# Kernel optimization log

Hardware: AMD Instinct MI355X
Metric: run time of the kernel (lower is better)

The kernel has to match this reference:

```python
import jax, jax.numpy as jnp
import numpy as np

TOPK = 30  # from init_kwargs


def setup_inputs() -> dict:
    key = jax.random.key(0)
    k1, k2, k3 = jax.random.split(key, 3)
    BH, N, D = 32, 2048, 64  # (batch*heads, seq_len, head_dim)
    return {
        "q": jax.random.normal(k1, (BH, N, D), dtype=jnp.float32),
        "k": jax.random.normal(k2, (BH, N, D), dtype=jnp.float32),
        "v": jax.random.normal(k3, (BH, N, D), dtype=jnp.float32),
        "B": 2048,          # == seq_len N (used for mask shape in original)
        "num_heads": 8,     # unused by the math, kept for signature parity
    }


def reference(q, k, v, B, num_heads):
    # scores: [BH, N, N]  (torch.bmm(q, k.transpose(1,2)))
    scores = jnp.einsum('bnd,bmd->bnm', q, k)
    # scale=None and attn_mask=None in the default call -> both branches skipped
    BH, N, _ = scores.shape
    # top-k per row, scatter 1.0 into a zero mask (faithful to torch.scatter_)
    _, idx = jax.lax.top_k(scores, TOPK)                      # [BH, N, TOPK]
    bi = jnp.arange(BH)[:, None, None]
    ri = jnp.arange(N)[None, :, None]
    keep = jnp.zeros((BH, N, N), dtype=bool).at[bi, ri, idx].set(True)
    # masked softmax over last axis (dim=2)
    masked = jnp.where(keep, scores, -jnp.inf)
    attn = jax.nn.softmax(masked, axis=-1)
    # dropout p=0.0 -> identity
    context = jnp.einsum('bnm,bmd->bnd', attn, v)
    return context, attn
```

## Files before the change

kernel.cpp:

```cpp
#include <hip/hip_runtime.h>
#include <hip/hip_bf16.h>

#define BHn 32
#define Nn 2048
#define Dn 64
#define KSEL 30
#define CAP 112
#define RB 128
#define CT 64
#define ZTH 1.80f

typedef short bf16x8 __attribute__((ext_vector_type(8)));
typedef float f32x4 __attribute__((ext_vector_type(4)));
typedef unsigned long long u64;

__device__ __forceinline__ unsigned ford(float x) {
  unsigned b = __float_as_uint(x);
  return (b & 0x80000000u) ? ~b : (b | 0x80000000u);
}
__device__ __forceinline__ float unford(unsigned u) {
  unsigned b = (u & 0x80000000u) ? (u & 0x7fffffffu) : ~u;
  return __uint_as_float(b);
}
__device__ __forceinline__ u64 umax64(u64 a, u64 b) { return a > b ? a : b; }

__device__ __forceinline__ void split2(float a, float b, ushort2& hi, ushort2& lo) {
  __hip_bfloat162 h = __float22bfloat162_rn(make_float2(a, b));
  union { __hip_bfloat162 v; ushort2 u; } ch; ch.v = h;
  hi = ch.u;
  float2 hf = __bfloat1622float2(h);
  __hip_bfloat162 l = __float22bfloat162_rn(make_float2(a - hf.x, b - hf.y));
  union { __hip_bfloat162 v; ushort2 u; } cl; cl.v = l;
  lo = cl.u;
}

__global__ __launch_bounds__(256, 3) void score_cand(
    const float* __restrict__ q, const float* __restrict__ k,
    u64* __restrict__ cand, unsigned* __restrict__ counts) {
  __shared__ ushort qh[RB][64], ql[RB][64];
  __shared__ ushort kh[CT][64], kl[CT][64];
  __shared__ unsigned ccnt[RB];
  __shared__ float tf[RB];

  const int t = threadIdx.x;
  const int bid = blockIdx.x;
  const int bh = (bid & 7) * 4 + ((bid >> 3) & 3);
  const int rb = bid >> 5;
  const int lane = t & 63, w = t >> 6;
  const int m16 = lane & 15, quad = lane >> 4;

  const float* qb = q + ((size_t)bh * Nn + rb * RB) * Dn;
  const float* kb = k + (size_t)bh * Nn * Dn;
  const size_t growbase = (size_t)bh * Nn + (size_t)rb * RB;

#pragma unroll
  for (int i = 0; i < 8; ++i) {
    int c = t + 256 * i;
    int row = c >> 4, f4 = c & 15;
    float4 a = *(const float4*)(qb + row * Dn + f4 * 4);
    int sp = (((f4 >> 1) ^ (row & 7)) << 1) | (f4 & 1);
    ushort2 h0, l0, h1, l1;
    split2(a.x, a.y, h0, l0);
    split2(a.z, a.w, h1, l1);
    *(ushort4*)&qh[row][sp * 4] = make_ushort4(h0.x, h0.y, h1.x, h1.y);
    *(ushort4*)&ql[row][sp * 4] = make_ushort4(l0.x, l0.y, l1.x, l1.y);
  }
  if (t < RB) {
    const float* qr = qb + t * Dn;
    float ss = 0.f;
#pragma unroll
    for (int i = 0; i < 16; ++i) {
      float4 a = *(const float4*)(qr + i * 4);
      ss = fmaf(a.x, a.x, ss); ss = fmaf(a.y, a.y, ss);
      ss = fmaf(a.z, a.z, ss); ss = fmaf(a.w, a.w, ss);
    }
    tf[t] = ZTH * sqrtf(ss);
    ccnt[t] = 0u;
  }

  unsigned tfr[2][4];
  float4 pre[4];
#pragma unroll
  for (int i = 0; i < 4; ++i) {
    int c = t + 256 * i;
    pre[i] = *(const float4*)(kb + (size_t)(c >> 4) * Dn + (c & 15) * 4);
  }
  __syncthreads();

#pragma unroll
  for (int mt = 0; mt < 2; ++mt)
#pragma unroll
    for (int rg = 0; rg < 4; ++rg)
      tfr[mt][rg] = ford(tf[w * 32 + mt * 16 + quad * 4 + rg]);

  for (int ct = 0; ct < Nn / CT; ++ct) {
#pragma unroll
    for (int i = 0; i < 4; ++i) {
      int c = t + 256 * i;
      int row = c >> 4, f4 = c & 15;
      float4 a = pre[i];
      int sp = (((f4 >> 1) ^ (row & 7)) << 1) | (f4 & 1);
      ushort2 h0, l0, h1, l1;
      split2(a.x, a.y, h0, l0);
      split2(a.z, a.w, h1, l1);
      *(ushort4*)&kh[row][sp * 4] = make_ushort4(h0.x, h0.y, h1.x, h1.y);
      *(ushort4*)&kl[row][sp * 4] = make_ushort4(l0.x, l0.y, l1.x, l1.y);
    }
    __syncthreads();

    if (ct + 1 < Nn / CT) {
#pragma unroll
      for (int i = 0; i < 4; ++i) {
        int c = t + 256 * i;
        pre[i] = *(const float4*)(kb + (size_t)((ct + 1) * CT + (c >> 4)) * Dn + (c & 15) * 4);
      }
    }

    f32x4 acc[2][4];
#pragma unroll
    for (int mt = 0; mt < 2; ++mt)
#pragma unroll
      for (int nt = 0; nt < 4; ++nt) acc[mt][nt] = (f32x4){0.f, 0.f, 0.f, 0.f};

#pragma unroll
    for (int ks = 0; ks < 2; ++ks) {
      bf16x8 aH[2], aL[2], bH[4], bL[4];
#pragma unroll
      for (int mt = 0; mt < 2; ++mt) {
        int r = w * 32 + mt * 16 + m16;
        int ch = (ks * 4 + quad) ^ (r & 7);
        aH[mt] = *(const bf16x8*)&qh[r][ch * 8];
        aL[mt] = *(const bf16x8*)&ql[r][ch * 8];
      }
#pragma unroll
      for (int nt = 0; nt < 4; ++nt) {
        int rr = nt * 16 + m16;
        int ch = (ks * 4 + quad) ^ (rr & 7);
        bH[nt] = *(const bf16x8*)&kh[rr][ch * 8];
        bL[nt] = *(const bf16x8*)&kl[rr][ch * 8];
      }
#pragma unroll
      for (int mt = 0; mt < 2; ++mt)
#pragma unroll
        for (int nt = 0; nt < 4; ++nt) {
          acc[mt][nt] = __builtin_amdgcn_mfma_f32_16x16x32_bf16(aL[mt], bH[nt], acc[mt][nt], 0, 0, 0);
          acc[mt][nt] = __builtin_amdgcn_mfma_f32_16x16x32_bf16(aH[mt], bL[nt], acc[mt][nt], 0, 0, 0);
          acc[mt][nt] = __builtin_amdgcn_mfma_f32_16x16x32_bf16(aH[mt], bH[nt], acc[mt][nt], 0, 0, 0);
        }
    }

#pragma unroll
    for (int mt = 0; mt < 2; ++mt)
#pragma unroll
      for (int rg = 0; rg < 4; ++rg) {
        unsigned tk = tfr[mt][rg];
        int rl = w * 32 + mt * 16 + quad * 4 + rg;
#pragma unroll
        for (int nt = 0; nt < 4; ++nt) {
          float s = acc[mt][nt][rg];
          unsigned fk = ford(s);
          if (fk > tk) {
            unsigned pos = atomicAdd(&ccnt[rl], 1u);
            if (pos < CAP) {
              int col = ct * CT + nt * 16 + m16;
              cand[(growbase + rl) * CAP + pos] =
                  ((u64)fk << 32) | (unsigned)(2047 - col);
            }
          }
        }
      }
    __syncthreads();
  }
  if (t < RB) counts[growbase + t] = ccnt[t];
}

__global__ __launch_bounds__(256) void select_fill(
    u64* __restrict__ cand, const unsigned* __restrict__ counts,
    const float* __restrict__ v, float* __restrict__ ctx,
    float* __restrict__ attn, unsigned* __restrict__ flags) {
  __shared__ float lrow[4 * Nn];
  __shared__ u64 scr[4][CAP];
  const int t = threadIdx.x;
  const int lane = t & 63, wv = t >> 6;
  const size_t row0 = (size_t)blockIdx.x * 4;
  const size_t gr = row0 + wv;
  const int bh = (int)(gr >> 11);

#pragma unroll
  for (int i = 0; i < 8; ++i)
    *(f32x4*)&lrow[i * 1024 + t * 4] = (f32x4){0.f, 0.f, 0.f, 0.f};

  const int C = (int)counts[gr];
  const bool bad = (C < KSEL) || (C > CAP);
  if (lane == 0) flags[gr] = bad ? 1u : 0u;

  if (!bad) {
    u64* sw_ = scr[wv];
    for (int p = lane; p < C; p += 64) sw_[p] = cand[gr * CAP + p];

    const int slots = (C + 63) >> 6;
    u64 mykey[2] = {0ull, 0ull};
    int rk[2] = {CAP, CAP};
    float es[2] = {0.f, 0.f};
    u64 mymax = 0ull;
#pragma unroll
    for (int tt = 0; tt < 2; ++tt) {
      if (tt < slots) {
        int p = lane + 64 * tt;
        mykey[tt] = (p < C) ? sw_[p] : 0ull;
        mymax = umax64(mymax, mykey[tt]);
      }
    }
#pragma unroll
    for (int off = 32; off; off >>= 1) mymax = umax64(mymax, __shfl_xor(mymax, off));
    const float mrow = unford((unsigned)(mymax >> 32));

#pragma unroll 1
    for (int tt = 0; tt < slots; ++tt) {
      int r = 0;
      u64 me = mykey[tt];
      for (int jj = 0; jj < C; ++jj) r += (sw_[jj] > me);
      rk[tt] = r;
    }
    float z = 0.f;
#pragma unroll
    for (int tt = 0; tt < 2; ++tt) {
      int p = lane + 64 * tt;
      bool sel = (tt < slots) && (p < C) && (rk[tt] < KSEL);
      es[tt] = sel ? __expf(unford((unsigned)(mykey[tt] >> 32)) - mrow) : 0.f;
      z += es[tt];
    }
#pragma unroll
    for (int off = 32; off; off >>= 1) z += __shfl_xor(z, off);
    const float invZ = 1.f / z;

#pragma unroll
    for (int tt = 0; tt < 2; ++tt) {
      int p = lane + 64 * tt;
      if (tt < slots && p < C && rk[tt] < KSEL) {
        float wt = es[tt] * invZ;
        int col = 2047 - (int)(mykey[tt] & 0xffffffffu);
        u64 e = ((u64)__float_as_uint(wt) << 32) | (unsigned)col;
        sw_[rk[tt]] = e;
        lrow[wv * Nn + col] = wt;
      }
    }
    const float* vb = v + (size_t)bh * Nn * Dn;
    float a = 0.f;
#pragma unroll
    for (int p = 0; p < KSEL; ++p) {
      u64 e = sw_[p];
      a = fmaf(__uint_as_float((unsigned)(e >> 32)), vb[(e & 0x7ffull) * Dn + lane], a);
    }
    ctx[gr * Dn + lane] = a;
  }
  __syncthreads();

  float* ab = attn + row0 * Nn;
#pragma unroll
  for (int i = 0; i < 8; ++i) {
    f32x4 vv = *(const f32x4*)&lrow[i * 1024 + t * 4];
    __builtin_nontemporal_store(vv, (f32x4*)(ab + i * 1024 + t * 4));
  }
}

__global__ __launch_bounds__(256) void repair_rows(
    const float* __restrict__ q, const float* __restrict__ k,
    const float* __restrict__ v, float* __restrict__ ctx,
    float* __restrict__ attn, const unsigned* __restrict__ flags) {
  __shared__ float sc2[Nn];
  __shared__ u64 red[256];
  __shared__ float qrow[Dn];
  __shared__ int selc[KSEL];
  __shared__ float selv[KSEL];
  __shared__ float zsh;
  __shared__ unsigned flagbuf[256];

  const int t = threadIdx.x;
  const int base = blockIdx.x * 256;
  flagbuf[t] = flags[base + t];
  __syncthreads();

  for (int i = 0; i < 256; ++i) {
    if (flagbuf[i] == 0u) continue;
    const int gr = base + i;
    const int bh = gr >> 11;
    if (t < Dn) qrow[t] = q[(size_t)gr * Dn + t];
    __syncthreads();
    const float* kb = k + (size_t)bh * Nn * Dn;
#pragma unroll
    for (int j = 0; j < 8; ++j) {
      int col = t + 256 * j;
      float s = 0.f;
      for (int d = 0; d < Dn; d += 4) {
        float4 kk = *(const float4*)(kb + (size_t)col * Dn + d);
        s = fmaf(qrow[d], kk.x, s);
        s = fmaf(qrow[d + 1], kk.y, s);
        s = fmaf(qrow[d + 2], kk.z, s);
        s = fmaf(qrow[d + 3], kk.w, s);
      }
      sc2[col] = s;
    }
    __syncthreads();
    for (int p = 0; p < KSEL; ++p) {
      u64 best = 0ull;
#pragma unroll
      for (int j = 0; j < 8; ++j) {
        int col = t + 256 * j;
        u64 kk = ((u64)ford(sc2[col]) << 32) | (unsigned)(2047 - col);
        best = umax64(best, kk);
      }
      red[t] = best;
      __syncthreads();
      for (int off = 128; off; off >>= 1) {
        if (t < off) red[t] = umax64(red[t], red[t + off]);
        __syncthreads();
      }
      if (t == 0) {
        u64 b = red[0];
        int col = 2047 - (int)(b & 0xffffffffu);
        selc[p] = col;
        selv[p] = unford((unsigned)(b >> 32));
        sc2[col] = -3.4e38f;
      }
      __syncthreads();
    }
    if (t == 0) {
      float m = selv[0], zz = 0.f;
      for (int p = 0; p < KSEL; ++p) zz += __expf(selv[p] - m);
      zsh = 1.f / zz;
    }
    __syncthreads();
    if (t < KSEL)
      attn[(size_t)gr * Nn + selc[t]] = __expf(selv[t] - selv[0]) * zsh;
    if (t < Dn) {
      const float* vb = v + (size_t)bh * Nn * Dn;
      float a = 0.f;
      for (int p = 0; p < KSEL; ++p)
        a = fmaf(__expf(selv[p] - selv[0]) * zsh, vb[(size_t)selc[p] * Dn + t], a);
      ctx[(size_t)gr * Dn + t] = a;
    }
    __syncthreads();
  }
}

extern "C" void kernel_launch(void* const* d_in, const int* in_sizes, int n_in,
                              void* d_out, int out_size, void* d_ws,
                              size_t ws_size, hipStream_t stream) {
  const float* q = (const float*)d_in[0];
  const float* k = (const float*)d_in[1];
  const float* v = (const float*)d_in[2];
  float* out = (float*)d_out;
  float* ctx = out;
  float* attn = out + (size_t)BHn * Nn * Dn;

  unsigned* counts = (unsigned*)d_ws;
  unsigned* flags = counts + (size_t)BHn * Nn;
  u64* cand = (u64*)((char*)d_ws + (size_t)BHn * Nn * 8);

  score_cand<<<dim3(BHn * Nn / RB), 256, 0, stream>>>(q, k, cand, counts);
  select_fill<<<dim3(BHn * Nn / 4), 256, 0, stream>>>(cand, counts, v, ctx, attn, flags);
  repair_rows<<<dim3(BHn * Nn / 256), 256, 0, stream>>>(q, k, v, ctx, attn, flags);
}
```

Measured before the change: 803.8 us.

## Fuse candidate scoring and top-k selection into one kernel with LDS candidate buffers

Merges the score/candidate kernel with the select-and-fill kernel, so candidates stay in shared memory and are never written to or read back from global workspace. Q fragments are held in registers instead of LDS. The row block shrinks to 64 and the 4 waves are split 2x2 over rows and columns. The threshold and capacity change (ZTH 1.90, CAP 92), and the attention row is written as zeros followed by scattered nontemporal stores of the weights. The risks are lower occupancy from the larger LDS candidate array, twice as many K reloads per row, an ordering dependency between the zero and weight stores guarded by a waitcnt, and possibly more rows sent to the repair path.

```diff
diff --git a/kernel.cpp b/kernel.cpp
--- a/kernel.cpp
+++ b/kernel.cpp
@@ -5,10 +5,10 @@
 #define Nn 2048
 #define Dn 64
 #define KSEL 30
-#define CAP 112
-#define RB 128
+#define CAP 92
+#define RB 64
 #define CT 64
-#define ZTH 1.80f
+#define ZTH 1.90f
 
 typedef short bf16x8 __attribute__((ext_vector_type(8)));
 typedef float f32x4 __attribute__((ext_vector_type(4)));
@@ -34,11 +34,22 @@
   lo = cl.u;
 }
 
-__global__ __launch_bounds__(256, 3) void score_cand(
+__device__ __forceinline__ void pack8(float4 x0, float4 x1, bf16x8& hi, bf16x8& lo) {
+  ushort2 h0, l0, h1, l1, h2, l2, h3, l3;
+  split2(x0.x, x0.y, h0, l0); split2(x0.z, x0.w, h1, l1);
+  split2(x1.x, x1.y, h2, l2); split2(x1.z, x1.w, h3, l3);
+  hi = (bf16x8){(short)h0.x, (short)h0.y, (short)h1.x, (short)h1.y,
+                (short)h2.x, (short)h2.y, (short)h3.x, (short)h3.y};
+  lo = (bf16x8){(short)l0.x, (short)l0.y, (short)l1.x, (short)l1.y,
+                (short)l2.x, (short)l2.y, (short)l3.x, (short)l3.y};
+}
+
+__global__ __launch_bounds__(256, 2) void score_select(
     const float* __restrict__ q, const float* __restrict__ k,
-    u64* __restrict__ cand, unsigned* __restrict__ counts) {
-  __shared__ ushort qh[RB][64], ql[RB][64];
+    const float* __restrict__ v, float* __restrict__ ctx,
+    float* __restrict__ attn, unsigned* __restrict__ flags) {
   __shared__ ushort kh[CT][64], kl[CT][64];
+  __shared__ u64 candL[RB][CAP];
   __shared__ unsigned ccnt[RB];
   __shared__ float tf[RB];
 
@@ -48,23 +59,23 @@
   const int rb = bid >> 5;
   const int lane = t & 63, w = t >> 6;
   const int m16 = lane & 15, quad = lane >> 4;
+  const int wr = w >> 1, wc = w & 1;
 
   const float* qb = q + ((size_t)bh * Nn + rb * RB) * Dn;
   const float* kb = k + (size_t)bh * Nn * Dn;
   const size_t growbase = (size_t)bh * Nn + (size_t)rb * RB;
 
-#pragma unroll
-  for (int i = 0; i < 8; ++i) {
-    int c = t + 256 * i;
-    int row = c >> 4, f4 = c & 15;
-    float4 a = *(const float4*)(qb + row * Dn + f4 * 4);
-    int sp = (((f4 >> 1) ^ (row & 7)) << 1) | (f4 & 1);
-    ushort2 h0, l0, h1, l1;
-    split2(a.x, a.y, h0, l0);
-    split2(a.z, a.w, h1, l1);
-    *(ushort4*)&qh[row][sp * 4] = make_ushort4(h0.x, h0.y, h1.x, h1.y);
-    *(ushort4*)&ql[row][sp * 4] = make_ushort4(l0.x, l0.y, l1.x, l1.y);
-  }
+  bf16x8 qaH[2][2], qaL[2][2];
+#pragma unroll
+  for (int ks = 0; ks < 2; ++ks)
+#pragma unroll
+    for (int mt = 0; mt < 2; ++mt) {
+      const float* p = qb + (wr * 32 + mt * 16 + m16) * Dn + (ks * 4 + quad) * 8;
+      float4 x0 = *(const float4*)p;
+      float4 x1 = *(const float4*)(p + 4);
+      pack8(x0, x1, qaH[ks][mt], qaL[ks][mt]);
+    }
+
   if (t < RB) {
     const float* qr = qb + t * Dn;
     float ss = 0.f;
@@ -78,7 +89,6 @@
     ccnt[t] = 0u;
   }
 
-  unsigned tfr[2][4];
   float4 pre[4];
 #pragma unroll
   for (int i = 0; i < 4; ++i) {
@@ -87,11 +97,12 @@
   }
   __syncthreads();
 
+  unsigned tfr[2][4];
 #pragma unroll
   for (int mt = 0; mt < 2; ++mt)
 #pragma unroll
     for (int rg = 0; rg < 4; ++rg)
-      tfr[mt][rg] = ford(tf[w * 32 + mt * 16 + quad * 4 + rg]);
+      tfr[mt][rg] = ford(tf[wr * 32 + mt * 16 + quad * 4 + rg]);
 
   for (int ct = 0; ct < Nn / CT; ++ct) {
 #pragma unroll
@@ -116,25 +127,18 @@
       }
     }
 
-    f32x4 acc[2][4];
+    f32x4 acc[2][2];
 #pragma unroll
     for (int mt = 0; mt < 2; ++mt)
 #pragma unroll
-      for (int nt = 0; nt < 4; ++nt) acc[mt][nt] = (f32x4){0.f, 0.f, 0.f, 0.f};
+      for (int nt = 0; nt < 2; ++nt) acc[mt][nt] = (f32x4){0.f, 0.f, 0.f, 0.f};
 
 #pragma unroll
     for (int ks = 0; ks < 2; ++ks) {
-      bf16x8 aH[2], aL[2], bH[4], bL[4];
-#pragma unroll
-      for (int mt = 0; mt < 2; ++mt) {
-        int r = w * 32 + mt * 16 + m16;
-        int ch = (ks * 4 + quad) ^ (r & 7);
-        aH[mt] = *(const bf16x8*)&qh[r][ch * 8];
-        aL[mt] = *(const bf16x8*)&ql[r][ch * 8];
-      }
-#pragma unroll
-      for (int nt = 0; nt < 4; ++nt) {
-        int rr = nt * 16 + m16;
+      bf16x8 bH[2], bL[2];
+#pragma unroll
+      for (int nt = 0; nt < 2; ++nt) {
+        int rr = wc * 32 + nt * 16 + m16;
         int ch = (ks * 4 + quad) ^ (rr & 7);
         bH[nt] = *(const bf16x8*)&kh[rr][ch * 8];
         bL[nt] = *(const bf16x8*)&kl[rr][ch * 8];
@@ -142,10 +146,10 @@
 #pragma unroll
       for (int mt = 0; mt < 2; ++mt)
 #pragma unroll
-        for (int nt = 0; nt < 4; ++nt) {
-          acc[mt][nt] = __builtin_amdgcn_mfma_f32_16x16x32_bf16(aL[mt], bH[nt], acc[mt][nt], 0, 0, 0);
-          acc[mt][nt] = __builtin_amdgcn_mfma_f32_16x16x32_bf16(aH[mt], bL[nt], acc[mt][nt], 0, 0, 0);
-          acc[mt][nt] = __builtin_amdgcn_mfma_f32_16x16x32_bf16(aH[mt], bH[nt], acc[mt][nt], 0, 0, 0);
+        for (int nt = 0; nt < 2; ++nt) {
+          acc[mt][nt] = __builtin_amdgcn_mfma_f32_16x16x32_bf16(qaL[ks][mt], bH[nt], acc[mt][nt], 0, 0, 0);
+          acc[mt][nt] = __builtin_amdgcn_mfma_f32_16x16x32_bf16(qaH[ks][mt], bL[nt], acc[mt][nt], 0, 0, 0);
+          acc[mt][nt] = __builtin_amdgcn_mfma_f32_16x16x32_bf16(qaH[ks][mt], bH[nt], acc[mt][nt], 0, 0, 0);
         }
     }
 
@@ -154,113 +158,103 @@
 #pragma unroll
       for (int rg = 0; rg < 4; ++rg) {
         unsigned tk = tfr[mt][rg];
-        int rl = w * 32 + mt * 16 + quad * 4 + rg;
-#pragma unroll
-        for (int nt = 0; nt < 4; ++nt) {
+        int rl = wr * 32 + mt * 16 + quad * 4 + rg;
+#pragma unroll
+        for (int nt = 0; nt < 2; ++nt) {
           float s = acc[mt][nt][rg];
           unsigned fk = ford(s);
           if (fk > tk) {
             unsigned pos = atomicAdd(&ccnt[rl], 1u);
             if (pos < CAP) {
-              int col = ct * CT + nt * 16 + m16;
-              cand[(growbase + rl) * CAP + pos] =
-                  ((u64)fk << 32) | (unsigned)(2047 - col);
+              int col = ct * CT + wc * 32 + nt * 16 + m16;
+              candL[rl][pos] = ((u64)fk << 32) | (unsigned)(2047 - col);
             }
           }
         }
       }
     __syncthreads();
   }
-  if (t < RB) counts[growbase + t] = ccnt[t];
-}
-
-__global__ __launch_bounds__(256) void select_fill(
-    u64* __restrict__ cand, const unsigned* __restrict__ counts,
-    const float* __restrict__ v, float* __restrict__ ctx,
-    float* __restrict__ attn, unsigned* __restrict__ flags) {
-  __shared__ float lrow[4 * Nn];
-  __shared__ u64 scr[4][CAP];
-  const int t = threadIdx.x;
-  const int lane = t & 63, wv = t >> 6;
-  const size_t row0 = (size_t)blockIdx.x * 4;
-  const size_t gr = row0 + wv;
-  const int bh = (int)(gr >> 11);
-
-#pragma unroll
-  for (int i = 0; i < 8; ++i)
-    *(f32x4*)&lrow[i * 1024 + t * 4] = (f32x4){0.f, 0.f, 0.f, 0.f};
-
-  const int C = (int)counts[gr];
-  const bool bad = (C < KSEL) || (C > CAP);
-  if (lane == 0) flags[gr] = bad ? 1u : 0u;
-
-  if (!bad) {
-    u64* sw_ = scr[wv];
-    for (int p = lane; p < C; p += 64) sw_[p] = cand[gr * CAP + p];
-
-    const int slots = (C + 63) >> 6;
-    u64 mykey[2] = {0ull, 0ull};
-    int rk[2] = {CAP, CAP};
-    float es[2] = {0.f, 0.f};
-    u64 mymax = 0ull;
-#pragma unroll
-    for (int tt = 0; tt < 2; ++tt) {
-      if (tt < slots) {
+
+  const float* vb = v + (size_t)bh * Nn * Dn;
+  for (int i = 0; i < RB / 4; ++i) {
+    const int rl = w * 16 + i;
+    const size_t gr = growbase + rl;
+    const int C = (int)ccnt[rl];
+    const bool bad = (C < KSEL) || (C > CAP);
+    if (lane == 0) flags[gr] = bad ? 1u : 0u;
+    float* ab = attn + gr * (size_t)Nn;
+
+    const f32x4 Z = (f32x4){0.f, 0.f, 0.f, 0.f};
+#pragma unroll
+    for (int jj = 0; jj < 8; ++jj)
+      __builtin_nontemporal_store(Z, (f32x4*)(ab + jj * 256 + lane * 4));
+
+    if (!bad) {
+      u64* sw_ = &candL[rl][0];
+      const int slots = (C + 63) >> 6;
+      u64 mykey[2] = {0ull, 0ull};
+      int rk[2] = {CAP, CAP};
+      float es[2] = {0.f, 0.f};
+      u64 mymax = 0ull;
+#pragma unroll
+      for (int tt = 0; tt < 2; ++tt) {
+        if (tt < slots) {
+          int p = lane + 64 * tt;
+          mykey[tt] = (p < C) ? sw_[p] : 0ull;
+          mymax = umax64(mymax, mykey[tt]);
+        }
+      }
+#pragma unroll
+      for (int off = 32; off; off >>= 1) mymax = umax64(mymax, __shfl_xor(mymax, off));
+      const float mrow = unford((unsigned)(mymax >> 32));
+
+#pragma unroll 1
+      for (int tt = 0; tt < slots; ++tt) {
+        int r = 0;
+        u64 me = mykey[tt];
+        for (int jj = 0; jj < C; ++jj) r += (sw_[jj] > me);
+        rk[tt] = r;
+      }
+      float z = 0.f;
+#pragma unroll
+      for (int tt = 0; tt < 2; ++tt) {
         int p = lane + 64 * tt;
-        mykey[tt] = (p < C) ? sw_[p] : 0ull;
-        mymax = umax64(mymax, mykey[tt]);
-      }
-    }
-#pragma unroll
-    for (int off = 32; off; off >>= 1) mymax = umax64(mymax, __shfl_xor(mymax, off));
-    const float mrow = unford((unsigned)(mymax >> 32));
-
-#pragma unroll 1
-    for (int tt = 0; tt < slots; ++tt) {
-      int r = 0;
-      u64 me = mykey[tt];
-      for (int jj = 0; jj < C; ++jj) r += (sw_[jj] > me);
-      rk[tt] = r;
-    }
-    float z = 0.f;
-#pragma unroll
-    for (int tt = 0; tt < 2; ++tt) {
-      int p = lane + 64 * tt;
-      bool sel = (tt < slots) && (p < C) && (rk[tt] < KSEL);
-      es[tt] = sel ? __expf(unford((unsigned)(mykey[tt] >> 32)) - mrow) : 0.f;
-      z += es[tt];
-    }
-#pragma unroll
-    for (int off = 32; off; off >>= 1) z += __shfl_xor(z, off);
-    const float invZ = 1.f / z;
-
-#pragma unroll
-    for (int tt = 0; tt < 2; ++tt) {
-      int p = lane + 64 * tt;
-      if (tt < slots && p < C && rk[tt] < KSEL) {
-        float wt = es[tt] * invZ;
-        int col = 2047 - (int)(mykey[tt] & 0xffffffffu);
-        u64 e = ((u64)__float_as_uint(wt) << 32) | (unsigned)col;
-        sw_[rk[tt]] = e;
-        lrow[wv * Nn + col] = wt;
-      }
-    }
-    const float* vb = v + (size_t)bh * Nn * Dn;
-    float a = 0.f;
-#pragma unroll
-    for (int p = 0; p < KSEL; ++p) {
-      u64 e = sw_[p];
-      a = fmaf(__uint_as_float((unsigned)(e >> 32)), vb[(e & 0x7ffull) * Dn + lane], a);
-    }
-    ctx[gr * Dn + lane] = a;
-  }
-  __syncthreads();
-
-  float* ab = attn + row0 * Nn;
-#pragma unroll
-  for (int i = 0; i < 8; ++i) {
-    f32x4 vv = *(const f32x4*)&lrow[i * 1024 + t * 4];
-    __builtin_nontemporal_store(vv, (f32x4*)(ab + i * 1024 + t * 4));
+        bool sel = (tt < slots) && (p < C) && (rk[tt] < KSEL);
+        es[tt] = sel ? __expf(unford((unsigned)(mykey[tt] >> 32)) - mrow) : 0.f;
+        z += es[tt];
+      }
+#pragma unroll
+      for (int off = 32; off; off >>= 1) z += __shfl_xor(z, off);
+      const float invZ = 1.f / z;
+
+#pragma unroll
+      for (int tt = 0; tt < 2; ++tt) {
+        int p = lane + 64 * tt;
+        if (tt < slots && p < C && rk[tt] < KSEL) {
+          float wt = es[tt] * invZ;
+          int col = 2047 - (int)(mykey[tt] & 0xffffffffu);
+          sw_[rk[tt]] = ((u64)__float_as_uint(wt) << 32) | (unsigned)col;
+        }
+      }
+      float a = 0.f;
+#pragma unroll
+      for (int p = 0; p < KSEL; ++p) {
+        u64 e = sw_[p];
+        a = fmaf(__uint_as_float((unsigned)(e >> 32)), vb[(e & 0x7ffull) * Dn + lane], a);
+      }
+      ctx[gr * Dn + lane] = a;
+
+      asm volatile("s_waitcnt vmcnt(0)" ::: "memory");
+#pragma unroll
+      for (int tt = 0; tt < 2; ++tt) {
+        int p = lane + 64 * tt;
+        if (tt < slots && p < C && rk[tt] < KSEL) {
+          float wt = es[tt] * invZ;
+          int col = 2047 - (int)(mykey[tt] & 0xffffffffu);
+          __builtin_nontemporal_store(wt, ab + col);
+        }
+      }
+    }
   }
 }
 
@@ -354,11 +348,8 @@
   float* ctx = out;
   float* attn = out + (size_t)BHn * Nn * Dn;
 
-  unsigned* counts = (unsigned*)d_ws;
-  unsigned* flags = counts + (size_t)BHn * Nn;
-  u64* cand = (u64*)((char*)d_ws + (size_t)BHn * Nn * 8);
-
-  score_cand<<<dim3(BHn * Nn / RB), 256, 0, stream>>>(q, k, cand, counts);
-  select_fill<<<dim3(BHn * Nn / 4), 256, 0, stream>>>(cand, counts, v, ctx, attn, flags);
+  unsigned* flags = (unsigned*)d_ws;
+
+  score_select<<<dim3(BHn * Nn / RB), 256, 0, stream>>>(q, k, v, ctx, attn, flags);
   repair_rows<<<dim3(BHn * Nn / 256), 256, 0, stream>>>(q, k, v, ctx, attn, flags);
 }
```

Result: slower. 881.3 us (+9.7%).
